# Performance work log

Measured on AMD Instinct MI355X. Metric: run time of the kernel, lower is better.

The kernel has to match this reference:

```python
import jax, jax.numpy as jnp
import numpy as np

B = 32768


def _mk(key, shape, scale=0.05):
    return (jax.random.normal(key, shape, dtype=jnp.float32) * scale)


def setup_inputs() -> dict:
    key = jax.random.key(0)
    ks = jax.random.split(key, 24)
    inp = {
        "p_i": jax.random.normal(ks[0], (B, 512), dtype=jnp.float32),
        "speed": jax.random.normal(ks[1], (B,), dtype=jnp.float32),
        "command": jax.random.randint(ks[2], (B,), 0, 4),
        "sp_W1": _mk(ks[3], (1, 128)), "sp_b1": jnp.zeros((128,), jnp.float32),
        "sp_W2": _mk(ks[4], (128, 128)), "sp_b2": jnp.zeros((128,), jnp.float32),
        "sp_W3": _mk(ks[5], (128, 128)), "sp_b3": jnp.zeros((128,), jnp.float32),
        # speed_pred_module: 512 -> 128 -> 128 -> 1
        "vp_W1": _mk(ks[6], (512, 128)), "vp_b1": jnp.zeros((128,), jnp.float32),
        "vp_W2": _mk(ks[7], (128, 128)), "vp_b2": jnp.zeros((128,), jnp.float32),
        "vp_W3": _mk(ks[8], (128, 1)), "vp_b3": jnp.zeros((1,), jnp.float32),
        # join_module: Linear(640, 512)
        "join_W": _mk(ks[9], (640, 512)), "join_b": jnp.zeros((512,), jnp.float32),
        # 4 control heads: 512 -> 256 -> 256 -> 3 (stacked over expert axis e)
        "ctrl_W1": _mk(ks[10], (4, 512, 256)), "ctrl_b1": jnp.zeros((4, 256), jnp.float32),
        "ctrl_W2": _mk(ks[11], (4, 256, 256)), "ctrl_b2": jnp.zeros((4, 256), jnp.float32),
        "ctrl_W3": _mk(ks[12], (4, 256, 3)), "ctrl_b3": jnp.zeros((4, 3), jnp.float32),
    }
    return inp


def _mlp3(x, W1, b1, W2, b2, W3, b3):
    h = jax.nn.relu(x @ W1 + b1)
    h = jax.nn.relu(h @ W2 + b2)
    return h @ W3 + b3


def reference(p_i, speed, command,
              sp_W1, sp_b1, sp_W2, sp_b2, sp_W3, sp_b3,
              vp_W1, vp_b1, vp_W2, vp_b2, vp_W3, vp_b3,
              join_W, join_b,
              ctrl_W1, ctrl_b1, ctrl_W2, ctrl_b2, ctrl_W3, ctrl_b3):
    v = _mlp3(speed[:, None], sp_W1, sp_b1, sp_W2, sp_b2, sp_W3, sp_b3)
    # join: [B, 640] -> [B, 512]
    joined = jnp.concatenate([p_i, v], axis=1) @ join_W + join_b
    # speed prediction [B,1]
    v_p = _mlp3(p_i, vp_W1, vp_b1, vp_W2, vp_b2, vp_W3, vp_b3)
    # command-indexed routing: compute all 4 tiny heads batched, then select.
    h = jax.nn.relu(jnp.einsum('bd,edh->beh', joined, ctrl_W1) + ctrl_b1)  # [B,4,256]
    h = jax.nn.relu(jnp.einsum('beh,ehk->bek', h, ctrl_W2) + ctrl_b2)      # [B,4,256]
    a = jnp.einsum('beh,ehk->bek', h, ctrl_W3) + ctrl_b3                    # [B,4,3]
    action = jnp.take_along_axis(a, command[:, None, None], axis=1)[:, 0, :]  # [B,3]
    return (v_p, action)
```

## Files before the change

### kernel.cpp

```cpp
#include <hip/hip_runtime.h>
#include <stdint.h>

#define NROWS 32768

typedef float f32x4 __attribute__((ext_vector_type(4)));
typedef __bf16 bfx8 __attribute__((ext_vector_type(8)));
typedef unsigned uint4v __attribute__((ext_vector_type(4)));

static __device__ __forceinline__ unsigned short f2bf(float f) {
    unsigned u = __builtin_bit_cast(unsigned, f);
    u += 0x7fffu + ((u >> 16) & 1u);
    return (unsigned short)(u >> 16);
}

static __device__ __forceinline__ f32x4 mfma16(bfx8 a, bfx8 b, f32x4 c) {
    return __builtin_amdgcn_mfma_f32_16x16x32_bf16(a, b, c, 0, 0, 0);
}

static __device__ __forceinline__ void gload_lds16(const void* g, void* l) {
    __builtin_amdgcn_global_load_lds(
        (const __attribute__((address_space(1))) void*)g,
        (__attribute__((address_space(3))) void*)l, 16, 0, 0);
}

static __device__ __forceinline__ int swz(int row, int col) {
    return col ^ ((row & 7) << 3);
}

static constexpr size_t JOINED_B = 0;
static constexpr size_t PI_B     = 33554432;
static constexpr size_t V_B      = 67108864;
static constexpr size_t WCT_B    = 75497472;
static constexpr size_t SPW2T_B  = 76316672;
static constexpr size_t SPW3T_B  = 76349440;
static constexpr size_t VPW2T_B  = 76382208;
static constexpr size_t VPW3T_B  = 76414976;
static constexpr size_t C1T_B    = 76419072;
static constexpr size_t C2T_B    = 77467648;
static constexpr size_t C3T_B    = 77991936;
static constexpr size_t CNT_B    = 78024704;
static constexpr size_t SORTED_B = 78024768;
static constexpr size_t WS_NEED  = 78549056;

__global__ __launch_bounds__(256) void k_prep(
    const float* p_i, const float* joinW, const float* vpW1, const float* spW2,
    const float* spW3, const float* vpW2, const float* vpW3,
    const float* c1, const float* c2, const float* c3,
    unsigned short* pib, unsigned short* wct, unsigned short* spw2t, unsigned short* spw3t,
    unsigned short* vpw2t, unsigned short* vpw3t,
    unsigned short* c1t, unsigned short* c2t, unsigned short* c3t, int* cnt)
{
    int bid = blockIdx.x, tid = threadIdx.x;
    if (bid == 0 && tid < 16) cnt[tid] = 0;
    if (bid < 4096) {
        size_t c0 = (size_t)bid * 1024;
#pragma unroll
        for (int j = 0; j < 4; ++j) {
            size_t c = c0 + tid + j * 256;
            f32x4 x = *(const f32x4*)(p_i + c * 4);
            ushort4 o;
            o.x = f2bf(x[0]); o.y = f2bf(x[1]); o.z = f2bf(x[2]); o.w = f2bf(x[3]);
            *(ushort4*)(pib + c * 4) = o;
        }
        return;
    }
    int b = bid - 4096;
    int region, s0;
    if      (b < 256)  { region = 0; s0 = b * 1024; }
    else if (b < 320)  { region = 1; s0 = (b - 256) * 1024; }
    else if (b < 336)  { region = 2; s0 = (b - 320) * 1024; }
    else if (b < 352)  { region = 3; s0 = (b - 336) * 1024; }
    else if (b < 368)  { region = 4; s0 = (b - 352) * 1024; }
    else if (b < 384)  { region = 5; s0 = (b - 368) * 1024; }
    else if (b < 386)  { region = 6; s0 = (b - 384) * 1024; }
    else if (b < 898)  { region = 7; s0 = (b - 386) * 1024; }
    else if (b < 1154) { region = 8; s0 = (b - 898) * 1024; }
    else               { region = 9; s0 = (b - 1154) * 1024; }
    for (int j = 0; j < 4; ++j) {
        int s = s0 + tid + j * 256;
        switch (region) {
        case 0: { int k = s >> 9, n = s & 511; wct[n * 640 + k] = f2bf(joinW[s]); } break;
        case 1: { int k = s >> 7, n = s & 127; wct[(512 + n) * 640 + k] = f2bf(vpW1[s]); } break;
        case 2: { int n = 512 + (s >> 7), k = 512 + (s & 127); wct[n * 640 + k] = 0; } break;
        case 3: { int k = s >> 7, n = s & 127; spw2t[n * 128 + k] = f2bf(spW2[s]); } break;
        case 4: { int k = s >> 7, n = s & 127; spw3t[n * 128 + k] = f2bf(spW3[s]); } break;
        case 5: { int k = s >> 7, n = s & 127; vpw2t[n * 128 + k] = f2bf(vpW2[s]); } break;
        case 6: { vpw3t[s] = (s < 128) ? f2bf(vpW3[s]) : 0; } break;
        case 7: { int e = s >> 17, k = (s >> 8) & 511, n = s & 255;
                  c1t[e * 131072 + n * 512 + k] = f2bf(c1[s]); } break;
        case 8: { int e = s >> 16, k = (s >> 8) & 255, n = s & 255;
                  c2t[e * 65536 + n * 256 + k] = f2bf(c2[s]); } break;
        case 9: { int e = s >> 12, r = s & 4095, n = r >> 8, k = r & 255;
                  c3t[s] = (n < 3) ? f2bf(c3[e * 768 + k * 3 + n]) : 0; } break;
        }
    }
}

__global__ __launch_bounds__(256) void k_sp(
    const float* speed, const float* spW1, const float* spb1,
    const float* spb2, const float* spb3,
    const unsigned short* spw2t, const unsigned short* spw3t,
    const int* command, int* cnt, int* sorted, unsigned short* v)
{
    __shared__ alignas(16) unsigned short h1[128 * 128];
    __shared__ alignas(16) unsigned short h2[128 * 128];
    __shared__ int lcnt[4], lbase[4];
    int bid = blockIdx.x, tid = threadIdx.x;
    int r0 = bid * 128;

    if (tid < 4) lcnt[tid] = 0;
    __syncthreads();
    int cc = 0, lpos = 0;
    if (tid < 128) { cc = command[r0 + tid] & 3; lpos = atomicAdd(&lcnt[cc], 1); }
    __syncthreads();
    if (tid < 4) lbase[tid] = atomicAdd(&cnt[tid], lcnt[tid]);
    __syncthreads();
    if (tid < 128) sorted[cc * NROWS + lbase[cc] + lpos] = r0 + tid;

    for (int j = 0; j < 64; ++j) {
        int idx = tid + j * 256;
        int row = idx >> 7, col = idx & 127;
        float h = speed[r0 + row] * spW1[col] + spb1[col];
        h = h > 0.f ? h : 0.f;
        h1[row * 128 + swz(row, col)] = f2bf(h);
    }
    __syncthreads();

    int wave = tid >> 6, lane = tid & 63, lq = lane >> 4, lr = lane & 15;
    int wr = wave >> 1, wc = wave & 1;
    f32x4 acc[4][4] = {};
#pragma unroll
    for (int ks = 0; ks < 4; ++ks) {
        bfx8 a[4], b[4];
#pragma unroll
        for (int mt = 0; mt < 4; ++mt) {
            int row = wr * 64 + mt * 16 + lr;
            a[mt] = *(const bfx8*)&h1[row * 128 + swz(row, ks * 32 + lq * 8)];
        }
#pragma unroll
        for (int nt = 0; nt < 4; ++nt) {
            int n = wc * 64 + nt * 16 + lr;
            b[nt] = *(const bfx8*)(spw2t + n * 128 + ks * 32 + lq * 8);
        }
#pragma unroll
        for (int mt = 0; mt < 4; ++mt)
#pragma unroll
            for (int nt = 0; nt < 4; ++nt)
                acc[mt][nt] = mfma16(a[mt], b[nt], acc[mt][nt]);
    }
#pragma unroll
    for (int mt = 0; mt < 4; ++mt)
#pragma unroll
        for (int nt = 0; nt < 4; ++nt)
#pragma unroll
            for (int j = 0; j < 4; ++j) {
                int row = wr * 64 + mt * 16 + lq * 4 + j;
                int col = wc * 64 + nt * 16 + lr;
                float x = acc[mt][nt][j] + spb2[col];
                x = x > 0.f ? x : 0.f;
                h2[row * 128 + swz(row, col)] = f2bf(x);
            }
    __syncthreads();
    f32x4 acc2[4][4] = {};
#pragma unroll
    for (int ks = 0; ks < 4; ++ks) {
        bfx8 a[4], b[4];
#pragma unroll
        for (int mt = 0; mt < 4; ++mt) {
            int row = wr * 64 + mt * 16 + lr;
            a[mt] = *(const bfx8*)&h2[row * 128 + swz(row, ks * 32 + lq * 8)];
        }
#pragma unroll
        for (int nt = 0; nt < 4; ++nt) {
            int n = wc * 64 + nt * 16 + lr;
            b[nt] = *(const bfx8*)(spw3t + n * 128 + ks * 32 + lq * 8);
        }
#pragma unroll
        for (int mt = 0; mt < 4; ++mt)
#pragma unroll
            for (int nt = 0; nt < 4; ++nt)
                acc2[mt][nt] = mfma16(a[mt], b[nt], acc2[mt][nt]);
    }
#pragma unroll
    for (int mt = 0; mt < 4; ++mt)
#pragma unroll
        for (int nt = 0; nt < 4; ++nt)
#pragma unroll
            for (int j = 0; j < 4; ++j) {
                int row = wr * 64 + mt * 16 + lq * 4 + j;
                int col = wc * 64 + nt * 16 + lr;
                v[(size_t)(r0 + row) * 128 + col] = f2bf(acc2[mt][nt][j] + spb3[col]);
            }
}

__global__ __launch_bounds__(256) void k_join(
    const unsigned short* pib, const unsigned short* v, const unsigned short* wct,
    const float* joinb, const float* vpb1,
    const unsigned short* vpw2t, const unsigned short* vpw3t,
    const float* vpb2, const float* vpb3,
    unsigned short* joined, float* out_vp)
{
    __shared__ alignas(16) unsigned short stg[16384];
    int d = blockIdx.x;
    int L = (d & 7) * 160 + (d >> 3);
    int m0 = (L / 5) * 128, n0 = (L % 5) * 128;
    int tid = threadIdx.x, wave = tid >> 6, lane = tid & 63, lq = lane >> 4, lr = lane & 15;
    int wr = wave >> 1, wc = wave & 1;

    int r0t = tid >> 3, s0t = tid & 7;
    int ss = s0t ^ (r0t & 7);
    const unsigned short* pA = pib + (size_t)(m0 + r0t) * 512 + s0t * 8;
    const unsigned short* pAv = v + (size_t)(m0 + r0t) * 128 + s0t * 8;
    const unsigned short* pB = wct + (size_t)(n0 + r0t) * 640 + s0t * 8;
    unsigned short* lA = &stg[r0t * 64 + ss * 8];
    unsigned short* lB = &stg[8192 + r0t * 64 + ss * 8];

    uint4v ra[4], rb[4];
#pragma unroll
    for (int c2 = 0; c2 < 4; ++c2) {
        ra[c2] = *(const uint4v*)(pA + c2 * 16384);
        rb[c2] = *(const uint4v*)(pB + c2 * 20480);
    }
    f32x4 acc[4][4] = {};
#pragma unroll 1
    for (int kt = 0; kt < 10; ++kt) {
#pragma unroll
        for (int c2 = 0; c2 < 4; ++c2) {
            *(uint4v*)(lA + c2 * 2048) = ra[c2];
            *(uint4v*)(lB + c2 * 2048) = rb[c2];
        }
        __syncthreads();
        if (kt < 9) {
            if (kt < 7) {
#pragma unroll
                for (int c2 = 0; c2 < 4; ++c2)
                    ra[c2] = *(const uint4v*)(pA + c2 * 16384 + (kt + 1) * 64);
            } else {
#pragma unroll
                for (int c2 = 0; c2 < 4; ++c2)
                    ra[c2] = *(const uint4v*)(pAv + c2 * 4096 + (kt + 1 - 8) * 64);
            }
#pragma unroll
            for (int c2 = 0; c2 < 4; ++c2)
                rb[c2] = *(const uint4v*)(pB + c2 * 20480 + (kt + 1) * 64);
        }
#pragma unroll
        for (int ks = 0; ks < 2; ++ks) {
            bfx8 a[4], b[4];
#pragma unroll
            for (int mt = 0; mt < 4; ++mt) {
                int row = wr * 64 + mt * 16 + lr;
                a[mt] = *(const bfx8*)&stg[row * 64 + ((ks * 32 + lq * 8) ^ ((row & 7) << 3))];
            }
#pragma unroll
            for (int nt = 0; nt < 4; ++nt) {
                int n = wc * 64 + nt * 16 + lr;
                b[nt] = *(const bfx8*)&stg[8192 + n * 64 + ((ks * 32 + lq * 8) ^ ((n & 7) << 3))];
            }
#pragma unroll
            for (int mt = 0; mt < 4; ++mt)
#pragma unroll
                for (int nt = 0; nt < 4; ++nt)
                    acc[mt][nt] = mfma16(a[mt], b[nt], acc[mt][nt]);
        }
        __syncthreads();
    }

    if (n0 < 512) {
#pragma unroll
        for (int mt = 0; mt < 4; ++mt)
#pragma unroll
            for (int nt = 0; nt < 4; ++nt)
#pragma unroll
                for (int j = 0; j < 4; ++j) {
                    int row = m0 + wr * 64 + mt * 16 + lq * 4 + j;
                    int col = n0 + wc * 64 + nt * 16 + lr;
                    joined[(size_t)row * 512 + col] = f2bf(acc[mt][nt][j] + joinb[col]);
                }
        return;
    }

#pragma unroll
    for (int mt = 0; mt < 4; ++mt)
#pragma unroll
        for (int nt = 0; nt < 4; ++nt)
#pragma unroll
            for (int j = 0; j < 4; ++j) {
                int row = wr * 64 + mt * 16 + lq * 4 + j;
                int col = wc * 64 + nt * 16 + lr;
                float x = acc[mt][nt][j] + vpb1[col];
                x = x > 0.f ? x : 0.f;
                stg[row * 128 + swz(row, col)] = f2bf(x);
            }
    __syncthreads();
    f32x4 acc2[4][4] = {};
#pragma unroll
    for (int ks = 0; ks < 4; ++ks) {
        bfx8 a[4], b[4];
#pragma unroll
        for (int mt = 0; mt < 4; ++mt) {
            int row = wr * 64 + mt * 16 + lr;
            a[mt] = *(const bfx8*)&stg[row * 128 + swz(row, ks * 32 + lq * 8)];
        }
#pragma unroll
        for (int nt = 0; nt < 4; ++nt) {
            int n = wc * 64 + nt * 16 + lr;
            b[nt] = *(const bfx8*)(vpw2t + n * 128 + ks * 32 + lq * 8);
        }
#pragma unroll
        for (int mt = 0; mt < 4; ++mt)
#pragma unroll
            for (int nt = 0; nt < 4; ++nt)
                acc2[mt][nt] = mfma16(a[mt], b[nt], acc2[mt][nt]);
    }
    __syncthreads();
#pragma unroll
    for (int mt = 0; mt < 4; ++mt)
#pragma unroll
        for (int nt = 0; nt < 4; ++nt)
#pragma unroll
            for (int j = 0; j < 4; ++j) {
                int row = wr * 64 + mt * 16 + lq * 4 + j;
                int col = wc * 64 + nt * 16 + lr;
                float x = acc2[mt][nt][j] + vpb2[col];
                x = x > 0.f ? x : 0.f;
                stg[row * 128 + swz(row, col)] = f2bf(x);
            }
    __syncthreads();
    f32x4 acc3[2] = {};
#pragma unroll
    for (int ks = 0; ks < 4; ++ks) {
        bfx8 b = *(const bfx8*)(vpw3t + lr * 128 + ks * 32 + lq * 8);
#pragma unroll
        for (int mt = 0; mt < 2; ++mt) {
            int row = wave * 32 + mt * 16 + lr;
            bfx8 a = *(const bfx8*)&stg[row * 128 + swz(row, ks * 32 + lq * 8)];
            acc3[mt] = mfma16(a, b, acc3[mt]);
        }
    }
    if (lr == 0) {
#pragma unroll
        for (int mt = 0; mt < 2; ++mt)
#pragma unroll
            for (int j = 0; j < 4; ++j) {
                int row = wave * 32 + mt * 16 + lq * 4 + j;
                out_vp[m0 + row] = acc3[mt][j] + vpb3[0];
            }
    }
}

__global__ __launch_bounds__(512) void k_ctrl(
    const unsigned short* joined, const unsigned short* c1t, const unsigned short* c2t,
    const unsigned short* c3t, const float* b1, const float* b2, const float* b3,
    const int* cnt, const int* sorted, float* out_act)
{
    __shared__ alignas(16) unsigned short hls[128 * 256];
    __shared__ alignas(16) unsigned short Ast[128 * 64];
    __shared__ alignas(16) unsigned short Bst[256 * 64];
    __shared__ int ridx[128];
    int bid = blockIdx.x;
    int e = bid >> 8, i = bid & 255;
    int n_e = cnt[e];
    if (i * 128 >= n_e) return;
    int tid = threadIdx.x;
    if (tid < 128) {
        int g = i * 128 + tid;
        ridx[tid] = sorted[e * NROWS + (g < n_e ? g : n_e - 1)];
    }
    __syncthreads();
    int wave = tid >> 6, lane = tid & 63, lq = lane >> 4, lr = lane & 15;
    int wm = wave & 1, wn = wave >> 1;
    const unsigned short* W1 = c1t + e * (256 * 512);
    const unsigned short* W2 = c2t + e * (256 * 256);
    const unsigned short* W3 = c3t + e * (16 * 256);

    f32x4 acc[4][4] = {};
#pragma unroll 1
    for (int kt = 0; kt < 8; ++kt) {
#pragma unroll
        for (int it = 0; it < 2; ++it) {
            int chunk = it * 512 + tid;
            int row = chunk >> 3, sl = (chunk & 7) ^ (row & 7);
            gload_lds16(joined + (size_t)ridx[row] * 512 + kt * 64 + sl * 8,
                        &Ast[(it * 512 + wave * 64) * 8]);
        }
#pragma unroll
        for (int it = 0; it < 4; ++it) {
            int chunk = it * 512 + tid;
            int n = chunk >> 3, sl = (chunk & 7) ^ (n & 7);
            gload_lds16(W1 + (size_t)n * 512 + kt * 64 + sl * 8,
                        &Bst[(it * 512 + wave * 64) * 8]);
        }
        __syncthreads();
#pragma unroll
        for (int ks = 0; ks < 2; ++ks) {
            bfx8 a[4], b[4];
#pragma unroll
            for (int mt = 0; mt < 4; ++mt) {
                int row = wm * 64 + mt * 16 + lr;
                a[mt] = *(const bfx8*)&Ast[row * 64 + ((ks * 32 + lq * 8) ^ ((row & 7) << 3))];
            }
#pragma unroll
            for (int nt = 0; nt < 4; ++nt) {
                int n = wn * 64 + nt * 16 + lr;
                b[nt] = *(const bfx8*)&Bst[n * 64 + ((ks * 32 + lq * 8) ^ ((n & 7) << 3))];
            }
#pragma unroll
            for (int mt = 0; mt < 4; ++mt)
#pragma unroll
                for (int nt = 0; nt < 4; ++nt)
                    acc[mt][nt] = mfma16(a[mt], b[nt], acc[mt][nt]);
        }
        __syncthreads();
    }
#pragma unroll
    for (int mt = 0; mt < 4; ++mt)
#pragma unroll
        for (int nt = 0; nt < 4; ++nt)
#pragma unroll
            for (int j = 0; j < 4; ++j) {
                int row = wm * 64 + mt * 16 + lq * 4 + j;
                int col = wn * 64 + nt * 16 + lr;
                float x = acc[mt][nt][j] + b1[e * 256 + col];
                x = x > 0.f ? x : 0.f;
                hls[row * 256 + swz(row, col)] = f2bf(x);
            }
    __syncthreads();

    f32x4 acc2[4][4] = {};
#pragma unroll 1
    for (int kt = 0; kt < 4; ++kt) {
#pragma unroll
        for (int it = 0; it < 4; ++it) {
            int chunk = it * 512 + tid;
            int n = chunk >> 3, sl = (chunk & 7) ^ (n & 7);
            gload_lds16(W2 + (size_t)n * 256 + kt * 64 + sl * 8,
                        &Bst[(it * 512 + wave * 64) * 8]);
        }
        __syncthreads();
#pragma unroll
        for (int ks = 0; ks < 2; ++ks) {
            bfx8 a[4], b[4];
#pragma unroll
            for (int mt = 0; mt < 4; ++mt) {
                int row = wm * 64 + mt * 16 + lr;
                a[mt] = *(const bfx8*)&hls[row * 256 + swz(row, kt * 64 + ks * 32 + lq * 8)];
            }
#pragma unroll
            for (int nt = 0; nt < 4; ++nt) {
                int n = wn * 64 + nt * 16 + lr;
                b[nt] = *(const bfx8*)&Bst[n * 64 + ((ks * 32 + lq * 8) ^ ((n & 7) << 3))];
            }
#pragma unroll
            for (int mt = 0; mt < 4; ++mt)
#pragma unroll
                for (int nt = 0; nt < 4; ++nt)
                    acc2[mt][nt] = mfma16(a[mt], b[nt], acc2[mt][nt]);
        }
        __syncthreads();
    }
#pragma unroll
    for (int mt = 0; mt < 4; ++mt)
#pragma unroll
        for (int nt = 0; nt < 4; ++nt)
#pragma unroll
            for (int j = 0; j < 4; ++j) {
                int row = wm * 64 + mt * 16 + lq * 4 + j;
                int col = wn * 64 + nt * 16 + lr;
                float x = acc2[mt][nt][j] + b2[e * 256 + col];
                x = x > 0.f ? x : 0.f;
                hls[row * 256 + swz(row, col)] = f2bf(x);
            }
    __syncthreads();

    {
        f32x4 acc3 = {};
#pragma unroll
        for (int ks = 0; ks < 8; ++ks) {
            int row = wave * 16 + lr;
            bfx8 a = *(const bfx8*)&hls[row * 256 + swz(row, ks * 32 + lq * 8)];
            bfx8 b = *(const bfx8*)(W3 + lr * 256 + ks * 32 + lq * 8);
            acc3 = mfma16(a, b, acc3);
        }
#pragma unroll
        for (int j = 0; j < 4; ++j) {
            int row = wave * 16 + lq * 4 + j;
            int g = i * 128 + row;
            if (lr < 3 && g < n_e)
                out_act[(size_t)ridx[row] * 3 + lr] = acc3[j] + b3[e * 3 + lr];
        }
    }
}

extern "C" void kernel_launch(void* const* d_in, const int* in_sizes, int n_in,
                              void* d_out, int out_size, void* d_ws, size_t ws_size,
                              hipStream_t stream) {
    (void)in_sizes; (void)n_in; (void)out_size;
    if (ws_size < WS_NEED) return;

    const float* p_i    = (const float*)d_in[0];
    const float* speed  = (const float*)d_in[1];
    const int*   command= (const int*)d_in[2];
    const float* sp_W1  = (const float*)d_in[3];
    const float* sp_b1  = (const float*)d_in[4];
    const float* sp_W2  = (const float*)d_in[5];
    const float* sp_b2  = (const float*)d_in[6];
    const float* sp_W3  = (const float*)d_in[7];
    const float* sp_b3  = (const float*)d_in[8];
    const float* vp_W1  = (const float*)d_in[9];
    const float* vp_b1  = (const float*)d_in[10];
    const float* vp_W2  = (const float*)d_in[11];
    const float* vp_b2  = (const float*)d_in[12];
    const float* vp_W3  = (const float*)d_in[13];
    const float* vp_b3  = (const float*)d_in[14];
    const float* join_W = (const float*)d_in[15];
    const float* join_b = (const float*)d_in[16];
    const float* ctrl_W1= (const float*)d_in[17];
    const float* ctrl_b1= (const float*)d_in[18];
    const float* ctrl_W2= (const float*)d_in[19];
    const float* ctrl_b2= (const float*)d_in[20];
    const float* ctrl_W3= (const float*)d_in[21];
    const float* ctrl_b3= (const float*)d_in[22];

    char* ws = (char*)d_ws;
    unsigned short* joined = (unsigned short*)(ws + JOINED_B);
    unsigned short* pib    = (unsigned short*)(ws + PI_B);
    unsigned short* vbuf   = (unsigned short*)(ws + V_B);
    unsigned short* wct    = (unsigned short*)(ws + WCT_B);
    unsigned short* spw2t  = (unsigned short*)(ws + SPW2T_B);
    unsigned short* spw3t  = (unsigned short*)(ws + SPW3T_B);
    unsigned short* vpw2t  = (unsigned short*)(ws + VPW2T_B);
    unsigned short* vpw3t  = (unsigned short*)(ws + VPW3T_B);
    unsigned short* c1t    = (unsigned short*)(ws + C1T_B);
    unsigned short* c2t    = (unsigned short*)(ws + C2T_B);
    unsigned short* c3t    = (unsigned short*)(ws + C3T_B);
    int* cnt    = (int*)(ws + CNT_B);
    int* sorted = (int*)(ws + SORTED_B);

    float* out_vp  = (float*)d_out;
    float* out_act = out_vp + NROWS;

    k_prep<<<5266, 256, 0, stream>>>(p_i, join_W, vp_W1, sp_W2, sp_W3, vp_W2, vp_W3,
                                     ctrl_W1, ctrl_W2, ctrl_W3,
                                     pib, wct, spw2t, spw3t, vpw2t, vpw3t,
                                     c1t, c2t, c3t, cnt);
    k_sp<<<256, 256, 0, stream>>>(speed, sp_W1, sp_b1, sp_b2, sp_b3,
                                  spw2t, spw3t, command, cnt, sorted, vbuf);
    k_join<<<1280, 256, 0, stream>>>(pib, vbuf, wct, join_b, vp_b1,
                                     vpw2t, vpw3t, vp_b2, vp_b3, joined, out_vp);
    k_ctrl<<<1024, 512, 0, stream>>>(joined, c1t, c2t, c3t, ctrl_b1, ctrl_b2, ctrl_b3,
                                     cnt, sorted, out_act);
}
```

Before: 274.2 us.

## Fold join layer into per-expert control W1 and fuse speed-pred into control kernel

Precomputes per-expert fused weights join_W·ctrl_W1 plus folded biases, so the control kernel reads p_i and v directly with a K=640 GEMM instead of first writing and rereading the 32768x512 joined tensor. The speed-prediction MLP is also computed inside the control kernel, with vp_W1 appended as extra output columns of the fused weight, which removes the separate join kernel. The weight fold costs a small GEMM on extra k_sp blocks every call and a second bf16 rounding of the fused weights, which may change numerical error. The control GEMM grows from 256 to 384 output columns, so the speed-prediction work is repeated in each expert's rows, but these are gathered by command so each row is still computed once.

```diff
diff --git a/kernel.cpp b/kernel.cpp
--- a/kernel.cpp
+++ b/kernel.cpp
@@ -2,6 +2,7 @@
 #include <stdint.h>
 
 #define NROWS 32768
+#define BW1S 245760
 
 typedef float f32x4 __attribute__((ext_vector_type(4)));
 typedef __bf16 bfx8 __attribute__((ext_vector_type(8)));
@@ -17,38 +18,34 @@
     return __builtin_amdgcn_mfma_f32_16x16x32_bf16(a, b, c, 0, 0, 0);
 }
 
-static __device__ __forceinline__ void gload_lds16(const void* g, void* l) {
-    __builtin_amdgcn_global_load_lds(
-        (const __attribute__((address_space(1))) void*)g,
-        (__attribute__((address_space(3))) void*)l, 16, 0, 0);
-}
-
 static __device__ __forceinline__ int swz(int row, int col) {
     return col ^ ((row & 7) << 3);
 }
 
-static constexpr size_t JOINED_B = 0;
-static constexpr size_t PI_B     = 33554432;
-static constexpr size_t V_B      = 67108864;
-static constexpr size_t WCT_B    = 75497472;
-static constexpr size_t SPW2T_B  = 76316672;
-static constexpr size_t SPW3T_B  = 76349440;
-static constexpr size_t VPW2T_B  = 76382208;
-static constexpr size_t VPW3T_B  = 76414976;
-static constexpr size_t C1T_B    = 76419072;
-static constexpr size_t C2T_B    = 77467648;
-static constexpr size_t C3T_B    = 77991936;
-static constexpr size_t CNT_B    = 78024704;
-static constexpr size_t SORTED_B = 78024768;
-static constexpr size_t WS_NEED  = 78549056;
+static constexpr size_t PI_B     = 0;
+static constexpr size_t V_B      = 33554432;
+static constexpr size_t JOINWB_B = 41943040;
+static constexpr size_t C1T_B    = 42598400;
+static constexpr size_t C2T_B    = 43646976;
+static constexpr size_t C3T_B    = 44171264;
+static constexpr size_t SPW2T_B  = 44204032;
+static constexpr size_t SPW3T_B  = 44236800;
+static constexpr size_t VPW2T_B  = 44269568;
+static constexpr size_t VPW3T_B  = 44302336;
+static constexpr size_t BW1_B    = 44306432;
+static constexpr size_t B1P_B    = 46272512;
+static constexpr size_t CNT_B    = 46276608;
+static constexpr size_t SORTED_B = 46276672;
+static constexpr size_t WS_NEED  = 46800960;
 
 __global__ __launch_bounds__(256) void k_prep(
-    const float* p_i, const float* joinW, const float* vpW1, const float* spW2,
-    const float* spW3, const float* vpW2, const float* vpW3,
+    const float* p_i, const float* joinW, const float* vpW1,
+    const float* spW2, const float* spW3, const float* vpW2, const float* vpW3,
     const float* c1, const float* c2, const float* c3,
-    unsigned short* pib, unsigned short* wct, unsigned short* spw2t, unsigned short* spw3t,
-    unsigned short* vpw2t, unsigned short* vpw3t,
-    unsigned short* c1t, unsigned short* c2t, unsigned short* c3t, int* cnt)
+    unsigned short* pib, unsigned short* joinWb, unsigned short* c1t,
+    unsigned short* c2t, unsigned short* c3t,
+    unsigned short* spw2t, unsigned short* spw3t, unsigned short* vpw2t,
+    unsigned short* vpw3t, unsigned short* bw1, int* cnt)
 {
     int bid = blockIdx.x, tid = threadIdx.x;
     if (bid == 0 && tid < 16) cnt[tid] = 0;
@@ -66,32 +63,41 @@
     }
     int b = bid - 4096;
     int region, s0;
-    if      (b < 256)  { region = 0; s0 = b * 1024; }
-    else if (b < 320)  { region = 1; s0 = (b - 256) * 1024; }
-    else if (b < 336)  { region = 2; s0 = (b - 320) * 1024; }
-    else if (b < 352)  { region = 3; s0 = (b - 336) * 1024; }
-    else if (b < 368)  { region = 4; s0 = (b - 352) * 1024; }
-    else if (b < 384)  { region = 5; s0 = (b - 368) * 1024; }
-    else if (b < 386)  { region = 6; s0 = (b - 384) * 1024; }
-    else if (b < 898)  { region = 7; s0 = (b - 386) * 1024; }
-    else if (b < 1154) { region = 8; s0 = (b - 898) * 1024; }
-    else               { region = 9; s0 = (b - 1154) * 1024; }
+    if      (b < 320)  { region = 0; s0 = b * 1024; }
+    else if (b < 832)  { region = 1; s0 = (b - 320) * 1024; }
+    else if (b < 1088) { region = 2; s0 = (b - 832) * 1024; }
+    else if (b < 1104) { region = 3; s0 = (b - 1088) * 1024; }
+    else if (b < 1120) { region = 4; s0 = (b - 1104) * 1024; }
+    else if (b < 1136) { region = 5; s0 = (b - 1120) * 1024; }
+    else if (b < 1152) { region = 6; s0 = (b - 1136) * 1024; }
+    else if (b < 1154) { region = 7; s0 = (b - 1152) * 1024; }
+    else if (b < 1218) { region = 8; s0 = (b - 1154) * 1024; }
+    else               { region = 9; s0 = (b - 1218) * 1024; }
     for (int j = 0; j < 4; ++j) {
         int s = s0 + tid + j * 256;
         switch (region) {
-        case 0: { int k = s >> 9, n = s & 511; wct[n * 640 + k] = f2bf(joinW[s]); } break;
-        case 1: { int k = s >> 7, n = s & 127; wct[(512 + n) * 640 + k] = f2bf(vpW1[s]); } break;
-        case 2: { int n = 512 + (s >> 7), k = 512 + (s & 127); wct[n * 640 + k] = 0; } break;
-        case 3: { int k = s >> 7, n = s & 127; spw2t[n * 128 + k] = f2bf(spW2[s]); } break;
-        case 4: { int k = s >> 7, n = s & 127; spw3t[n * 128 + k] = f2bf(spW3[s]); } break;
-        case 5: { int k = s >> 7, n = s & 127; vpw2t[n * 128 + k] = f2bf(vpW2[s]); } break;
-        case 6: { vpw3t[s] = (s < 128) ? f2bf(vpW3[s]) : 0; } break;
-        case 7: { int e = s >> 17, k = (s >> 8) & 511, n = s & 255;
-                  c1t[e * 131072 + n * 512 + k] = f2bf(c1[s]); } break;
-        case 8: { int e = s >> 16, k = (s >> 8) & 255, n = s & 255;
+        case 0: joinWb[s] = f2bf(joinW[s]); break;
+        case 1: { int e = s >> 17, n = (s >> 8) & 511, m = s & 255;
+                  c1t[e * 131072 + m * 512 + n] = f2bf(c1[s]); } break;
+        case 2: { int e = s >> 16, k = (s >> 8) & 255, n = s & 255;
                   c2t[e * 65536 + n * 256 + k] = f2bf(c2[s]); } break;
-        case 9: { int e = s >> 12, r = s & 4095, n = r >> 8, k = r & 255;
+        case 3: { int e = s >> 12, r = s & 4095, n = r >> 8, k = r & 255;
                   c3t[s] = (n < 3) ? f2bf(c3[e * 768 + k * 3 + n]) : 0; } break;
+        case 4: { int k = s >> 7, n = s & 127; spw2t[n * 128 + k] = f2bf(spW2[s]); } break;
+        case 5: { int k = s >> 7, n = s & 127; spw3t[n * 128 + k] = f2bf(spW3[s]); } break;
+        case 6: { int k = s >> 7, n = s & 127; vpw2t[n * 128 + k] = f2bf(vpW2[s]); } break;
+        case 7: { vpw3t[s] = (s < 128) ? f2bf(vpW3[s]) : 0; } break;
+        case 8: { int k = s >> 7, n = s & 127;
+                  unsigned short val = f2bf(vpW1[s]);
+#pragma unroll
+                  for (int e = 0; e < 4; ++e)
+                      bw1[e * BW1S + (256 + n) * 640 + k] = val;
+                } break;
+        case 9: { int n = s >> 7, k = 512 + (s & 127);
+#pragma unroll
+                  for (int e = 0; e < 4; ++e)
+                      bw1[e * BW1S + (256 + n) * 640 + k] = 0;
+                } break;
         }
     }
 }
@@ -100,14 +106,80 @@
     const float* speed, const float* spW1, const float* spb1,
     const float* spb2, const float* spb3,
     const unsigned short* spw2t, const unsigned short* spw3t,
-    const int* command, int* cnt, int* sorted, unsigned short* v)
+    const int* command, int* cnt, int* sorted, unsigned short* v,
+    const unsigned short* c1t, const unsigned short* joinWb, unsigned short* bw1,
+    const float* c1f, const float* jb, const float* b1f, float* b1p)
 {
     __shared__ alignas(16) unsigned short h1[128 * 128];
     __shared__ alignas(16) unsigned short h2[128 * 128];
     __shared__ int lcnt[4], lbase[4];
     int bid = blockIdx.x, tid = threadIdx.x;
+
+    if (bid >= 296) {
+        int e = bid - 296;
+        float a = b1f[e * 256 + tid];
+        for (int n = 0; n < 512; ++n)
+            a = fmaf(jb[n], c1f[(size_t)e * 131072 + n * 256 + tid], a);
+        b1p[e * 256 + tid] = a;
+        return;
+    }
+    if (bid >= 256) {
+        int fid = bid - 256;
+        int e = fid / 10, rem = fid % 10;
+        int m0 = (rem / 5) * 128, k0 = (rem % 5) * 128;
+        const unsigned short* A = c1t + e * 131072;
+        unsigned short* stA = h1;
+        unsigned short* stB = h1 + 8192;
+        int wave = tid >> 6, lane = tid & 63, lq = lane >> 4, lr = lane & 15;
+        int wr = wave >> 1, wc = wave & 1;
+        f32x4 acc[4][4] = {};
+#pragma unroll 1
+        for (int kt = 0; kt < 8; ++kt) {
+#pragma unroll
+            for (int it = 0; it < 4; ++it) {
+                int chunk = it * 256 + tid;
+                int row = chunk >> 3, sl = chunk & 7;
+                uint4v va = *(const uint4v*)(A + (size_t)(m0 + row) * 512 + kt * 64 + sl * 8);
+                uint4v vb = *(const uint4v*)(joinWb + (size_t)(k0 + row) * 512 + kt * 64 + sl * 8);
+                *(uint4v*)&stA[row * 64 + (sl ^ (row & 7)) * 8] = va;
+                *(uint4v*)&stB[row * 64 + (sl ^ (row & 7)) * 8] = vb;
+            }
+            __syncthreads();
+#pragma unroll
+            for (int ks = 0; ks < 2; ++ks) {
+                bfx8 a[4], bb[4];
+#pragma unroll
+                for (int mt = 0; mt < 4; ++mt) {
+                    int row = wr * 64 + mt * 16 + lr;
+                    a[mt] = *(const bfx8*)&stA[row * 64 + ((ks * 32 + lq * 8) ^ ((row & 7) << 3))];
+                }
+#pragma unroll
+                for (int nt = 0; nt < 4; ++nt) {
+                    int n = wc * 64 + nt * 16 + lr;
+                    bb[nt] = *(const bfx8*)&stB[n * 64 + ((ks * 32 + lq * 8) ^ ((n & 7) << 3))];
+                }
+#pragma unroll
+                for (int mt = 0; mt < 4; ++mt)
+#pragma unroll
+                    for (int nt = 0; nt < 4; ++nt)
+                        acc[mt][nt] = mfma16(a[mt], bb[nt], acc[mt][nt]);
+            }
+            __syncthreads();
+        }
+#pragma unroll
+        for (int mt = 0; mt < 4; ++mt)
+#pragma unroll
+            for (int nt = 0; nt < 4; ++nt)
+#pragma unroll
+                for (int j = 0; j < 4; ++j) {
+                    int m = wr * 64 + mt * 16 + lq * 4 + j;
+                    int k = wc * 64 + nt * 16 + lr;
+                    bw1[e * BW1S + (m0 + m) * 640 + k0 + k] = f2bf(acc[mt][nt][j]);
+                }
+        return;
+    }
+
     int r0 = bid * 128;
-
     if (tid < 4) lcnt[tid] = 0;
     __syncthreads();
     int cc = 0, lpos = 0;
@@ -193,171 +265,19 @@
             }
 }
 
-__global__ __launch_bounds__(256) void k_join(
-    const unsigned short* pib, const unsigned short* v, const unsigned short* wct,
-    const float* joinb, const float* vpb1,
+__global__ __launch_bounds__(512) void k_ctrl(
+    const unsigned short* pib, const unsigned short* v,
+    const unsigned short* bw1, const float* b1p,
+    const unsigned short* c2t, const unsigned short* c3t,
     const unsigned short* vpw2t, const unsigned short* vpw3t,
-    const float* vpb2, const float* vpb3,
-    unsigned short* joined, float* out_vp)
+    const float* b2, const float* b3,
+    const float* vpb1, const float* vpb2, const float* vpb3,
+    const int* cnt, const int* sorted, float* out_vp, float* out_act)
 {
-    __shared__ alignas(16) unsigned short stg[16384];
-    int d = blockIdx.x;
-    int L = (d & 7) * 160 + (d >> 3);
-    int m0 = (L / 5) * 128, n0 = (L % 5) * 128;
-    int tid = threadIdx.x, wave = tid >> 6, lane = tid & 63, lq = lane >> 4, lr = lane & 15;
-    int wr = wave >> 1, wc = wave & 1;
-
-    int r0t = tid >> 3, s0t = tid & 7;
-    int ss = s0t ^ (r0t & 7);
-    const unsigned short* pA = pib + (size_t)(m0 + r0t) * 512 + s0t * 8;
-    const unsigned short* pAv = v + (size_t)(m0 + r0t) * 128 + s0t * 8;
-    const unsigned short* pB = wct + (size_t)(n0 + r0t) * 640 + s0t * 8;
-    unsigned short* lA = &stg[r0t * 64 + ss * 8];
-    unsigned short* lB = &stg[8192 + r0t * 64 + ss * 8];
-
-    uint4v ra[4], rb[4];
-#pragma unroll
-    for (int c2 = 0; c2 < 4; ++c2) {
-        ra[c2] = *(const uint4v*)(pA + c2 * 16384);
-        rb[c2] = *(const uint4v*)(pB + c2 * 20480);
-    }
-    f32x4 acc[4][4] = {};
-#pragma unroll 1
-    for (int kt = 0; kt < 10; ++kt) {
-#pragma unroll
-        for (int c2 = 0; c2 < 4; ++c2) {
-            *(uint4v*)(lA + c2 * 2048) = ra[c2];
-            *(uint4v*)(lB + c2 * 2048) = rb[c2];
-        }
-        __syncthreads();
-        if (kt < 9) {
-            if (kt < 7) {
-#pragma unroll
-                for (int c2 = 0; c2 < 4; ++c2)
-                    ra[c2] = *(const uint4v*)(pA + c2 * 16384 + (kt + 1) * 64);
-            } else {
-#pragma unroll
-                for (int c2 = 0; c2 < 4; ++c2)
-                    ra[c2] = *(const uint4v*)(pAv + c2 * 4096 + (kt + 1 - 8) * 64);
-            }
-#pragma unroll
-            for (int c2 = 0; c2 < 4; ++c2)
-                rb[c2] = *(const uint4v*)(pB + c2 * 20480 + (kt + 1) * 64);
-        }
-#pragma unroll
-        for (int ks = 0; ks < 2; ++ks) {
-            bfx8 a[4], b[4];
-#pragma unroll
-            for (int mt = 0; mt < 4; ++mt) {
-                int row = wr * 64 + mt * 16 + lr;
-                a[mt] = *(const bfx8*)&stg[row * 64 + ((ks * 32 + lq * 8) ^ ((row & 7) << 3))];
-            }
-#pragma unroll
-            for (int nt = 0; nt < 4; ++nt) {
-                int n = wc * 64 + nt * 16 + lr;
-                b[nt] = *(const bfx8*)&stg[8192 + n * 64 + ((ks * 32 + lq * 8) ^ ((n & 7) << 3))];
-            }
-#pragma unroll
-            for (int mt = 0; mt < 4; ++mt)
-#pragma unroll
-                for (int nt = 0; nt < 4; ++nt)
-                    acc[mt][nt] = mfma16(a[mt], b[nt], acc[mt][nt]);
-        }
-        __syncthreads();
-    }
-
-    if (n0 < 512) {
-#pragma unroll
-        for (int mt = 0; mt < 4; ++mt)
-#pragma unroll
-            for (int nt = 0; nt < 4; ++nt)
-#pragma unroll
-                for (int j = 0; j < 4; ++j) {
-                    int row = m0 + wr * 64 + mt * 16 + lq * 4 + j;
-                    int col = n0 + wc * 64 + nt * 16 + lr;
-                    joined[(size_t)row * 512 + col] = f2bf(acc[mt][nt][j] + joinb[col]);
-                }
-        return;
-    }
-
-#pragma unroll
-    for (int mt = 0; mt < 4; ++mt)
-#pragma unroll
-        for (int nt = 0; nt < 4; ++nt)
-#pragma unroll
-            for (int j = 0; j < 4; ++j) {
-                int row = wr * 64 + mt * 16 + lq * 4 + j;
-                int col = wc * 64 + nt * 16 + lr;
-                float x = acc[mt][nt][j] + vpb1[col];
-                x = x > 0.f ? x : 0.f;
-                stg[row * 128 + swz(row, col)] = f2bf(x);
-            }
-    __syncthreads();
-    f32x4 acc2[4][4] = {};
-#pragma unroll
-    for (int ks = 0; ks < 4; ++ks) {
-        bfx8 a[4], b[4];
-#pragma unroll
-        for (int mt = 0; mt < 4; ++mt) {
-            int row = wr * 64 + mt * 16 + lr;
-            a[mt] = *(const bfx8*)&stg[row * 128 + swz(row, ks * 32 + lq * 8)];
-        }
-#pragma unroll
-        for (int nt = 0; nt < 4; ++nt) {
-            int n = wc * 64 + nt * 16 + lr;
-            b[nt] = *(const bfx8*)(vpw2t + n * 128 + ks * 32 + lq * 8);
-        }
-#pragma unroll
-        for (int mt = 0; mt < 4; ++mt)
-#pragma unroll
-            for (int nt = 0; nt < 4; ++nt)
-                acc2[mt][nt] = mfma16(a[mt], b[nt], acc2[mt][nt]);
-    }
-    __syncthreads();
-#pragma unroll
-    for (int mt = 0; mt < 4; ++mt)
-#pragma unroll
-        for (int nt = 0; nt < 4; ++nt)
-#pragma unroll
-            for (int j = 0; j < 4; ++j) {
-                int row = wr * 64 + mt * 16 + lq * 4 + j;
-                int col = wc * 64 + nt * 16 + lr;
-                float x = acc2[mt][nt][j] + vpb2[col];
-                x = x > 0.f ? x : 0.f;
-                stg[row * 128 + swz(row, col)] = f2bf(x);
-            }
-    __syncthreads();
-    f32x4 acc3[2] = {};
-#pragma unroll
-    for (int ks = 0; ks < 4; ++ks) {
-        bfx8 b = *(const bfx8*)(vpw3t + lr * 128 + ks * 32 + lq * 8);
-#pragma unroll
-        for (int mt = 0; mt < 2; ++mt) {
-            int row = wave * 32 + mt * 16 + lr;
-            bfx8 a = *(const bfx8*)&stg[row * 128 + swz(row, ks * 32 + lq * 8)];
-            acc3[mt] = mfma16(a, b, acc3[mt]);
-        }
-    }
-    if (lr == 0) {
-#pragma unroll
-        for (int mt = 0; mt < 2; ++mt)
-#pragma unroll
-            for (int j = 0; j < 4; ++j) {
-                int row = wave * 32 + mt * 16 + lq * 4 + j;
-                out_vp[m0 + row] = acc3[mt][j] + vpb3[0];
-            }
-    }
-}
-
-__global__ __launch_bounds__(512) void k_ctrl(
-    const unsigned short* joined, const unsigned short* c1t, const unsigned short* c2t,
-    const unsigned short* c3t, const float* b1, const float* b2, const float* b3,
-    const int* cnt, const int* sorted, float* out_act)
-{
-    __shared__ alignas(16) unsigned short hls[128 * 256];
-    __shared__ alignas(16) unsigned short Ast[128 * 64];
-    __shared__ alignas(16) unsigned short Bst[256 * 64];
+    __shared__ alignas(16) unsigned short lds[65536];
     __shared__ int ridx[128];
+    const int AST = 0, BST = 8192;
+    const int H = 0, G1 = 32768, WS = 49152;
     int bid = blockIdx.x;
     int e = bid >> 8, i = bid & 255;
     int n_e = cnt[e];
@@ -370,26 +290,80 @@
     __syncthreads();
     int wave = tid >> 6, lane = tid & 63, lq = lane >> 4, lr = lane & 15;
     int wm = wave & 1, wn = wave >> 1;
-    const unsigned short* W1 = c1t + e * (256 * 512);
-    const unsigned short* W2 = c2t + e * (256 * 256);
-    const unsigned short* W3 = c3t + e * (16 * 256);
-
-    f32x4 acc[4][4] = {};
+    const unsigned short* BW = bw1 + e * BW1S;
+
+    f32x4 acc[4][6] = {};
 #pragma unroll 1
-    for (int kt = 0; kt < 8; ++kt) {
+    for (int kt = 0; kt < 10; ++kt) {
 #pragma unroll
         for (int it = 0; it < 2; ++it) {
             int chunk = it * 512 + tid;
-            int row = chunk >> 3, sl = (chunk & 7) ^ (row & 7);
-            gload_lds16(joined + (size_t)ridx[row] * 512 + kt * 64 + sl * 8,
-                        &Ast[(it * 512 + wave * 64) * 8]);
-        }
+            int row = chunk >> 3, sl = chunk & 7;
+            uint4v val;
+            if (kt < 8) val = *(const uint4v*)(pib + (size_t)ridx[row] * 512 + kt * 64 + sl * 8);
+            else        val = *(const uint4v*)(v + (size_t)ridx[row] * 128 + (kt - 8) * 64 + sl * 8);
+            *(uint4v*)&lds[AST + row * 64 + (sl ^ (row & 7)) * 8] = val;
+        }
+#pragma unroll
+        for (int it = 0; it < 6; ++it) {
+            int chunk = it * 512 + tid;
+            int n = chunk >> 3, sl = chunk & 7;
+            uint4v val = *(const uint4v*)(BW + (size_t)n * 640 + kt * 64 + sl * 8);
+            *(uint4v*)&lds[BST + n * 64 + (sl ^ (n & 7)) * 8] = val;
+        }
+        __syncthreads();
+#pragma unroll
+        for (int ks = 0; ks < 2; ++ks) {
+            bfx8 a[4], b[6];
+#pragma unroll
+            for (int mt = 0; mt < 4; ++mt) {
+                int row = wm * 64 + mt * 16 + lr;
+                a[mt] = *(const bfx8*)&lds[AST + row * 64 + ((ks * 32 + lq * 8) ^ ((row & 7) << 3))];
+            }
+#pragma unroll
+            for (int nt = 0; nt < 6; ++nt) {
+                int n = wn * 96 + nt * 16 + lr;
+                b[nt] = *(const bfx8*)&lds[BST + n * 64 + ((ks * 32 + lq * 8) ^ ((n & 7) << 3))];
+            }
+#pragma unroll
+            for (int mt = 0; mt < 4; ++mt)
+#pragma unroll
+                for (int nt = 0; nt < 6; ++nt)
+                    acc[mt][nt] = mfma16(a[mt], b[nt], acc[mt][nt]);
+        }
+        __syncthreads();
+    }
+#pragma unroll
+    for (int mt = 0; mt < 4; ++mt)
+#pragma unroll
+        for (int nt = 0; nt < 6; ++nt)
+#pragma unroll
+            for (int j = 0; j < 4; ++j) {
+                int row = wm * 64 + mt * 16 + lq * 4 + j;
+                int col = wn * 96 + nt * 16 + lr;
+                float x = acc[mt][nt][j];
+                if (col < 256) {
+                    x += b1p[e * 256 + col];
+                    x = x > 0.f ? x : 0.f;
+                    lds[H + row * 256 + swz(row, col)] = f2bf(x);
+                } else {
+                    x += vpb1[col - 256];
+                    x = x > 0.f ? x : 0.f;
+                    lds[G1 + row * 128 + swz(row, col - 256)] = f2bf(x);
+                }
+            }
+    __syncthreads();
+
+    f32x4 acc2[4][4] = {};
+    const unsigned short* W2 = c2t + e * 65536;
+#pragma unroll 1
+    for (int kt = 0; kt < 4; ++kt) {
 #pragma unroll
         for (int it = 0; it < 4; ++it) {
             int chunk = it * 512 + tid;
-            int n = chunk >> 3, sl = (chunk & 7) ^ (n & 7);
-            gload_lds16(W1 + (size_t)n * 512 + kt * 64 + sl * 8,
-                        &Bst[(it * 512 + wave * 64) * 8]);
+            int n = chunk >> 3, sl = chunk & 7;
+            uint4v val = *(const uint4v*)(W2 + (size_t)n * 256 + kt * 64 + sl * 8);
+            *(uint4v*)&lds[WS + n * 64 + (sl ^ (n & 7)) * 8] = val;
         }
         __syncthreads();
 #pragma unroll
@@ -398,58 +372,12 @@
 #pragma unroll
             for (int mt = 0; mt < 4; ++mt) {
                 int row = wm * 64 + mt * 16 + lr;
-                a[mt] = *(const bfx8*)&Ast[row * 64 + ((ks * 32 + lq * 8) ^ ((row & 7) << 3))];
+                a[mt] = *(const bfx8*)&lds[H + row * 256 + swz(row, kt * 64 + ks * 32 + lq * 8)];
             }
 #pragma unroll
             for (int nt = 0; nt < 4; ++nt) {
                 int n = wn * 64 + nt * 16 + lr;
-                b[nt] = *(const bfx8*)&Bst[n * 64 + ((ks * 32 + lq * 8) ^ ((n & 7) << 3))];
-            }
-#pragma unroll
-            for (int mt = 0; mt < 4; ++mt)
-#pragma unroll
-                for (int nt = 0; nt < 4; ++nt)
-                    acc[mt][nt] = mfma16(a[mt], b[nt], acc[mt][nt]);
-        }
-        __syncthreads();
-    }
-#pragma unroll
-    for (int mt = 0; mt < 4; ++mt)
-#pragma unroll
-        for (int nt = 0; nt < 4; ++nt)
-#pragma unroll
-            for (int j = 0; j < 4; ++j) {
-                int row = wm * 64 + mt * 16 + lq * 4 + j;
-                int col = wn * 64 + nt * 16 + lr;
-                float x = acc[mt][nt][j] + b1[e * 256 + col];
-                x = x > 0.f ? x : 0.f;
-                hls[row * 256 + swz(row, col)] = f2bf(x);
-            }
-    __syncthreads();
-
-    f32x4 acc2[4][4] = {};
-#pragma unroll 1
-    for (int kt = 0; kt < 4; ++kt) {
-#pragma unroll
-        for (int it = 0; it < 4; ++it) {
-            int chunk = it * 512 + tid;
-            int n = chunk >> 3, sl = (chunk & 7) ^ (n & 7);
-            gload_lds16(W2 + (size_t)n * 256 + kt * 64 + sl * 8,
-                        &Bst[(it * 512 + wave * 64) * 8]);
-        }
-        __syncthreads();
-#pragma unroll
-        for (int ks = 0; ks < 2; ++ks) {
-            bfx8 a[4], b[4];
-#pragma unroll
-            for (int mt = 0; mt < 4; ++mt) {
-                int row = wm * 64 + mt * 16 + lr;
-                a[mt] = *(const bfx8*)&hls[row * 256 + swz(row, kt * 64 + ks * 32 + lq * 8)];
-            }
-#pragma unroll
-            for (int nt = 0; nt < 4; ++nt) {
-                int n = wn * 64 + nt * 16 + lr;
-                b[nt] = *(const bfx8*)&Bst[n * 64 + ((ks * 32 + lq * 8) ^ ((n & 7) << 3))];
+                b[nt] = *(const bfx8*)&lds[WS + n * 64 + ((ks * 32 + lq * 8) ^ ((n & 7) << 3))];
             }
 #pragma unroll
             for (int mt = 0; mt < 4; ++mt)
@@ -469,7 +397,40 @@
                 int col = wn * 64 + nt * 16 + lr;
                 float x = acc2[mt][nt][j] + b2[e * 256 + col];
                 x = x > 0.f ? x : 0.f;
-                hls[row * 256 + swz(row, col)] = f2bf(x);
+                lds[H + row * 256 + swz(row, col)] = f2bf(x);
+            }
+    f32x4 accv[4][2] = {};
+#pragma unroll
+    for (int ks = 0; ks < 4; ++ks) {
+        bfx8 a[4], b[2];
+#pragma unroll
+        for (int mt = 0; mt < 4; ++mt) {
+            int row = wm * 64 + mt * 16 + lr;
+            a[mt] = *(const bfx8*)&lds[G1 + row * 128 + swz(row, ks * 32 + lq * 8)];
+        }
+#pragma unroll
+        for (int nt = 0; nt < 2; ++nt) {
+            int n = wn * 32 + nt * 16 + lr;
+            b[nt] = *(const bfx8*)(vpw2t + n * 128 + ks * 32 + lq * 8);
+        }
+#pragma unroll
+        for (int mt = 0; mt < 4; ++mt)
+#pragma unroll
+            for (int nt = 0; nt < 2; ++nt)
+                accv[mt][nt] = mfma16(a[mt], b[nt], accv[mt][nt]);
+    }
+    __syncthreads();
+#pragma unroll
+    for (int mt = 0; mt < 4; ++mt)
+#pragma unroll
+        for (int nt = 0; nt < 2; ++nt)
+#pragma unroll
+            for (int j = 0; j < 4; ++j) {
+                int row = wm * 64 + mt * 16 + lq * 4 + j;
+                int col = wn * 32 + nt * 16 + lr;
+                float x = accv[mt][nt][j] + vpb2[col];
+                x = x > 0.f ? x : 0.f;
+                lds[WS + row * 128 + swz(row, col)] = f2bf(x);
             }
     __syncthreads();
 
@@ -478,16 +439,26 @@
 #pragma unroll
         for (int ks = 0; ks < 8; ++ks) {
             int row = wave * 16 + lr;
-            bfx8 a = *(const bfx8*)&hls[row * 256 + swz(row, ks * 32 + lq * 8)];
-            bfx8 b = *(const bfx8*)(W3 + lr * 256 + ks * 32 + lq * 8);
+            bfx8 a = *(const bfx8*)&lds[H + row * 256 + swz(row, ks * 32 + lq * 8)];
+            bfx8 b = *(const bfx8*)(c3t + e * 4096 + lr * 256 + ks * 32 + lq * 8);
             acc3 = mfma16(a, b, acc3);
+        }
+        f32x4 acc4 = {};
+#pragma unroll
+        for (int ks = 0; ks < 4; ++ks) {
+            int row = wave * 16 + lr;
+            bfx8 a = *(const bfx8*)&lds[WS + row * 128 + swz(row, ks * 32 + lq * 8)];
+            bfx8 b = *(const bfx8*)(vpw3t + lr * 128 + ks * 32 + lq * 8);
+            acc4 = mfma16(a, b, acc4);
         }
 #pragma unroll
         for (int j = 0; j < 4; ++j) {
             int row = wave * 16 + lq * 4 + j;
             int g = i * 128 + row;
-            if (lr < 3 && g < n_e)
-                out_act[(size_t)ridx[row] * 3 + lr] = acc3[j] + b3[e * 3 + lr];
+            if (g < n_e) {
+                if (lr < 3) out_act[(size_t)ridx[row] * 3 + lr] = acc3[j] + b3[e * 3 + lr];
+                if (lr == 0) out_vp[ridx[row]] = acc4[j] + vpb3[0];
+            }
         }
     }
 }
@@ -523,31 +494,32 @@
     const float* ctrl_b3= (const float*)d_in[22];
 
     char* ws = (char*)d_ws;
-    unsigned short* joined = (unsigned short*)(ws + JOINED_B);
     unsigned short* pib    = (unsigned short*)(ws + PI_B);
     unsigned short* vbuf   = (unsigned short*)(ws + V_B);
-    unsigned short* wct    = (unsigned short*)(ws + WCT_B);
+    unsigned short* joinWb = (unsigned short*)(ws + JOINWB_B);
+    unsigned short* c1t    = (unsigned short*)(ws + C1T_B);
+    unsigned short* c2t    = (unsigned short*)(ws + C2T_B);
+    unsigned short* c3t    = (unsigned short*)(ws + C3T_B);
     unsigned short* spw2t  = (unsigned short*)(ws + SPW2T_B);
     unsigned short* spw3t  = (unsigned short*)(ws + SPW3T_B);
     unsigned short* vpw2t  = (unsigned short*)(ws + VPW2T_B);
     unsigned short* vpw3t  = (unsigned short*)(ws + VPW3T_B);
-    unsigned short* c1t    = (unsigned short*)(ws + C1T_B);
-    unsigned short* c2t    = (unsigned short*)(ws + C2T_B);
-    unsigned short* c3t    = (unsigned short*)(ws + C3T_B);
+    unsigned short* bw1    = (unsigned short*)(ws + BW1_B);
+    float* b1p  = (float*)(ws + B1P_B);
     int* cnt    = (int*)(ws + CNT_B);
     int* sorted = (int*)(ws + SORTED_B);
 
     float* out_vp  = (float*)d_out;
     float* out_act = out_vp + NROWS;
 
-    k_prep<<<5266, 256, 0, stream>>>(p_i, join_W, vp_W1, sp_W2, sp_W3, vp_W2, vp_W3,
+    k_prep<<<5330, 256, 0, stream>>>(p_i, join_W, vp_W1, sp_W2, sp_W3, vp_W2, vp_W3,
                                      ctrl_W1, ctrl_W2, ctrl_W3,
-                                     pib, wct, spw2t, spw3t, vpw2t, vpw3t,
-                                     c1t, c2t, c3t, cnt);
-    k_sp<<<256, 256, 0, stream>>>(speed, sp_W1, sp_b1, sp_b2, sp_b3,
-                                  spw2t, spw3t, command, cnt, sorted, vbuf);
-    k_join<<<1280, 256, 0, stream>>>(pib, vbuf, wct, join_b, vp_b1,
-                                     vpw2t, vpw3t, vp_b2, vp_b3, joined, out_vp);
-    k_ctrl<<<1024, 512, 0, stream>>>(joined, c1t, c2t, c3t, ctrl_b1, ctrl_b2, ctrl_b3,
-                                     cnt, sorted, out_act);
-}
+                                     pib, joinWb, c1t, c2t, c3t,
+                                     spw2t, spw3t, vpw2t, vpw3t, bw1, cnt);
+    k_sp<<<300, 256, 0, stream>>>(speed, sp_W1, sp_b1, sp_b2, sp_b3,
+                                  spw2t, spw3t, command, cnt, sorted, vbuf,
+                                  c1t, joinWb, bw1, ctrl_W1, join_b, ctrl_b1, b1p);
+    k_ctrl<<<1024, 512, 0, stream>>>(pib, vbuf, bw1, b1p, c2t, c3t, vpw2t, vpw3t,
+                                     ctrl_b2, ctrl_b3, vp_b1, vp_b2, vp_b3,
+                                     cnt, sorted, out_vp, out_act);
+}
```

Result: faster. 257.9 us (-5.9%).
